# Performance work log

Hardware: AMD Instinct MI355X
Metric: run time of the kernel (lower is better)

## Reference

```python
import jax, jax.numpy as jnp
import numpy as np
import math

D_MODEL = 512
N_HEADS = 4
ANCHOR_PERIODS = [12, 24, 48, 96]
MIN_PERIOD = 4


def compute_periods(x, k=2, min_period=MIN_PERIOD):
    # x: [B, T, C] -> per-channel top-k ACF periods [C, k] (torch code runs this under no_grad)
    B, T, C = x.shape
    xc = x - x.mean(axis=1, keepdims=True)
    n_fft = 1 << (2 * T - 1).bit_length()
    xf = jnp.fft.rfft(xc, n=n_fft, axis=1)
    acf = jnp.fft.irfft(xf * jnp.conj(xf), n=n_fft, axis=1)[:, :T, :]
    avg = acf.mean(axis=0)  # [T, C]
    neg = jnp.array(-jnp.inf, avg.dtype)
    avg = avg.at[:min_period, :].set(neg)
    prev = jnp.roll(avg, 1, axis=0)
    nxt = jnp.roll(avg, -1, axis=0)
    is_peak = (avg > prev) & (avg > nxt) & (avg > 0)
    masked = jnp.where(is_peak, avg, neg)
    _, inds = jax.lax.top_k(masked.T, k)  # [C, k], top over lag axis
    return jnp.clip(inds, min_period, T // 2)


def _interp_matrix(new_len, old_len):
    # rows of F.interpolate(eye, size=(new_len, old_len), mode='bilinear', align_corners=False)
    j = np.arange(new_len, dtype=np.float64)
    src = np.clip((j + 0.5) * old_len / new_len - 0.5, 0.0, old_len - 1)
    i0 = np.floor(src).astype(np.int64)
    i1 = np.minimum(i0 + 1, old_len - 1)
    w = src - i0
    M = np.zeros((new_len, old_len), np.float32)
    M[np.arange(new_len), i0] += (1.0 - w).astype(np.float32)
    M[np.arange(new_len), i1] += w.astype(np.float32)
    return M


def flex_weight(anchors, target_len):
    nearest = min(ANCHOR_PERIODS, key=lambda p: abs(p - target_len))
    old = anchors[nearest]  # [d, nearest]
    if nearest == target_len:
        return old
    M = _interp_matrix(target_len, nearest)          # [new, old]
    Mpinv = jnp.asarray(np.linalg.pinv(M.T))          # pinv(resize_mat.T): [new, old]
    return (Mpinv @ old.T).T * math.sqrt(target_len / nearest)  # [d, new]


def attentive_agg(tokens, in_w, in_b, out_w, out_b, ln_g, ln_b):
    # tokens: [N, P, d]; MHA(query=last patch, key=value=all patches), eval mode (dropout=identity)
    N, P, d = tokens.shape
    hd = d // N_HEADS
    q = tokens[:, -1:, :]  # [N, 1, d]
    Wq, Wk, Wv = jnp.split(in_w, 3, axis=0)
    bq, bk, bv = jnp.split(in_b, 3)

    def heads(t, W, b):
        y = t @ W.T + b
        return y.reshape(N, t.shape[1], N_HEADS, hd).transpose(0, 2, 1, 3)

    Q = heads(q, Wq, bq)       # [N, H, 1, hd]
    K = heads(tokens, Wk, bk)  # [N, H, P, hd]
    V = heads(tokens, Wv, bv)
    attn = jax.nn.softmax(jnp.einsum('nhqe,nhke->nhqk', Q, K) / math.sqrt(hd), axis=-1)
    o = jnp.einsum('nhqk,nhke->nhqe', attn, V).transpose(0, 2, 1, 3).reshape(N, 1, d)
    o = o @ out_w.T + out_b
    y = q + o
    mu = y.mean(-1, keepdims=True)
    var = y.var(-1, keepdims=True)
    y = (y - mu) * jax.lax.rsqrt(var + 1e-5) * ln_g + ln_b
    return y[:, 0, :]


def setup_inputs() -> dict:
    key = jax.random.key(0)
    ks = jax.random.split(key, 16)
    B, T, C, d = 16, 384, 128, D_MODEL

    def xavier(k, shape):
        lim = math.sqrt(6.0 / (shape[0] + shape[1]))
        return jax.random.uniform(k, shape, jnp.float32, -lim, lim)

    inp = {'x': jax.random.normal(ks[0], (B, T, C), jnp.float32)}
    for i, p in enumerate(ANCHOR_PERIODS):
        inp[f'anchor_w{p}'] = xavier(ks[1 + i], (d, p))
    inp['shared_bias'] = jnp.zeros((d,), jnp.float32)
    for j, tag in enumerate(['agg1', 'agg2']):
        inp[f'{tag}_in_w'] = xavier(ks[5 + 2 * j], (3 * d, d))
        inp[f'{tag}_in_b'] = jnp.zeros((3 * d,), jnp.float32)
        inp[f'{tag}_out_w'] = xavier(ks[6 + 2 * j], (d, d))
        inp[f'{tag}_out_b'] = jnp.zeros((d,), jnp.float32)
        inp[f'{tag}_ln_g'] = jnp.ones((d,), jnp.float32)
        inp[f'{tag}_ln_b'] = jnp.zeros((d,), jnp.float32)
    inp['fusion_w1'] = xavier(ks[9], (d, 3 * d))
    inp['fusion_b1'] = jnp.zeros((d,), jnp.float32)
    inp['fusion_w2'] = xavier(ks[10], (d, d))
    inp['fusion_b2'] = jnp.zeros((d,), jnp.float32)
    return inp


def reference(x, anchor_w12, anchor_w24, anchor_w48, anchor_w96, shared_bias,
              agg1_in_w, agg1_in_b, agg1_out_w, agg1_out_b, agg1_ln_g, agg1_ln_b,
              agg2_in_w, agg2_in_b, agg2_out_w, agg2_out_b, agg2_ln_g, agg2_ln_b,
              fusion_w1, fusion_b1, fusion_w2, fusion_b2):
    B, T, C = x.shape
    d = D_MODEL
    periods = np.asarray(jax.device_get(compute_periods(x)))  # [C, 2] (no-grad routing)
    anchors = {12: anchor_w12, 24: anchor_w24, 48: anchor_w48, 96: anchor_w96}
    x_inv = jnp.transpose(x, (0, 2, 1))  # [B, C, T]

    w_trend = flex_weight(anchors, T)
    trend = x_inv @ w_trend.T + shared_bias  # [B, C, d]

    s1 = jnp.zeros((B, C, d), x.dtype)
    s2 = jnp.zeros((B, C, d), x.dtype)
    agg1 = (agg1_in_w, agg1_in_b, agg1_out_w, agg1_out_b, agg1_ln_g, agg1_ln_b)
    agg2 = (agg2_in_w, agg2_in_b, agg2_out_w, agg2_out_b, agg2_ln_g, agg2_ln_b)

    for p in np.unique(periods):
        p = int(p)
        m1 = periods[:, 0] == p
        m2 = periods[:, 1] == p
        tgt_idx = np.where(m1 | m2)[0]
        if tgt_idx.size == 0:
            continue
        w_p = flex_weight(anchors, p)
        num_p = T // p
        # unfold(size=p, step=p) == contiguous reshape of the first num_p*p samples
        patches = x_inv[:, tgt_idx, :num_p * p].reshape(B, tgt_idx.size, num_p, p)
        tokens = patches @ w_p.T + shared_bias  # [B, Csub, num_p, d]
        for m, aggp, slot in ((m1, agg1, 0), (m2, agg2, 1)):
            idx = np.where(m)[0]
            if idx.size == 0:
                continue
            rel = np.isin(tgt_idx, idx)
            sub = tokens[:, rel].reshape(-1, num_p, d)
            res = attentive_agg(sub, *aggp).reshape(B, idx.size, d)
            if slot == 0:
                s1 = s1.at[:, idx, :].set(res)
            else:
                s2 = s2.at[:, idx, :].set(res)

    combined = jnp.concatenate([s1, s2, trend], axis=-1)  # [B, C, 3d]
    h = jax.nn.gelu(combined @ fusion_w1.T + fusion_b1, approximate=False)
    return h @ fusion_w2.T + fusion_b2  # [B, C, d] (final dropout = identity in eval)
```

## Files before the change

kernel.cpp:

```cpp
#include <hip/hip_runtime.h>
#include <math.h>

#define Bn 16
#define Tn 384
#define Cn 128

static constexpr long OFF_XT   = 0;
static constexpr long OFF_AVG  = 786432;
static constexpr long OFF_PER  = 835584;
static constexpr long OFF_MP   = 835840;
static constexpr long OFF_AT   = 2507140;
static constexpr long OFF_WAF  = 2605444;
static constexpr long OFF_QAT  = 3195268;
static constexpr long OFF_VAT  = 3391876;
static constexpr long OFF_OVT  = 3588484;
static constexpr long OFF_CON  = 4374916;
static constexpr long OFF_VB   = 4377988;
static constexpr long OFF_MT   = 4379012;
static constexpr long OFF_DEF  = 4673924;
static constexpr long OFF_ZC   = 4677004;
static constexpr long OFF_COMB = 6643084;
static constexpr long OFF_H    = 9788812;
static constexpr long OFF_H2   = 10837388;
static constexpr long WS_FLOATS = 11885964;
// ... 307 lines not shown
      float v = part + inb[r];
      if (r < 1024) cons[s * 1536 + r] = v;
      else vbuf[s * 512 + (r - 1024)] = v;
    }
  }
}

__global__ __launch_bounds__(256) void prep1(const float* __restrict__ a12,
                                             const float* __restrict__ a24,
                                             const float* __restrict__ a48,
                                             const float* __restrict__ a96,
                                             const float* __restrict__ i1w,
                                             const float* __restrict__ i1b,
                                             const float* __restrict__ i2w,
                                             const float* __restrict__ i2b,
                                             const float* __restrict__ sb,
                                             float* __restrict__ at_tab,
                                             float* __restrict__ cons,
                                             float* __restrict__ vbuf) {
  __shared__ float sm[64 * 97];
  int bid = blockIdx.x;
  if (bid < 32) at_body(bid, a12, a24, a48, a96, at_tab, sm);
  else constsA_body(bid - 32, i1w, i1b, i2w, i2b, sb, cons, vbuf, sm);
}

__global__ __launch_bounds__(256) void wa_gemm2(const float* __restrict__ iw0,
                                                const float* __restrict__ iw1,
                                                const float* __restrict__ atb,
                                                float* __restrict__ waf,
                                                float* __restrict__ qat,
                                                float* __restrict__ vat) {
  __shared__ float smem[2 * 32 * 68];
  float* As = smem;
  float* Ws = smem + 32 * 68;
  int bid = blockIdx.x;
  int s = bid / 72, r = bid % 72;
  int m0 = (r / 3) * 64, n0 = (r % 3) * 64;
  const float* A = s ? iw1 : iw0;
  float* wafs = waf + (long)s * 294912;
  int tid = threadIdx.x;
  int tm = tid & 15, tn = tid >> 4;
  float acc[4][4];
#pragma unroll
  for (int i = 0; i < 4; ++i)
#pragma unroll
    for (int j = 0; j < 4; ++j) acc[i][j] = 0.f;
  int row = tid >> 3, kc = (tid & 7) * 4;
  for (int k0 = 0; k0 < 512; k0 += 32) {
    float4 v = *(const float4*)&A[(long)(m0 + row) * 512 + k0 + kc];
    As[(kc + 0) * 68 + row] = v.x; As[(kc + 1) * 68 + row] = v.y;
    As[(kc + 2) * 68 + row] = v.z; As[(kc + 3) * 68 + row] = v.w;
    v = *(const float4*)&A[(long)(m0 + row + 32) * 512 + k0 + kc];
    As[(kc + 0) * 68 + row + 32] = v.x; As[(kc + 1) * 68 + row + 32] = v.y;
    As[(kc + 2) * 68 + row + 32] = v.z; As[(kc + 3) * 68 + row + 32] = v.w;
    v = *(const float4*)&atb[(long)(n0 + row) * 512 + k0 + kc];
    Ws[(kc + 0) * 68 + row] = v.x; Ws[(kc + 1) * 68 + row] = v.y;
    Ws[(kc + 2) * 68 + row] = v.z; Ws[(kc + 3) * 68 + row] = v.w;
    v = *(const float4*)&atb[(long)(n0 + row + 32) * 512 + k0 + kc];
    Ws[(kc + 0) * 68 + row + 32] = v.x; Ws[(kc + 1) * 68 + row + 32] = v.y;
    Ws[(kc + 2) * 68 + row + 32] = v.z; Ws[(kc + 3) * 68 + row + 32] = v.w;
    __syncthreads();
    for (int kk = 0; kk < 32; ++kk) {
      float4 a = *(const float4*)&As[kk * 68 + tm * 4];
      float4 w = *(const float4*)&Ws[kk * 68 + tn * 4];
      acc[0][0] += a.x * w.x; acc[0][1] += a.x * w.y; acc[0][2] += a.x * w.z; acc[0][3] += a.x * w.w;
      acc[1][0] += a.y * w.x; acc[1][1] += a.y * w.y; acc[1][2] += a.y * w.z; acc[1][3] += a.y * w.w;
      acc[2][0] += a.z * w.x; acc[2][1] += a.z * w.y; acc[2][2] += a.z * w.z; acc[2][3] += a.z * w.w;
      acc[3][0] += a.w * w.x; acc[3][1] += a.w * w.y; acc[3][2] += a.w * w.z; acc[3][3] += a.w * w.w;
    }
    __syncthreads();
  }
#pragma unroll
  for (int mi = 0; mi < 4; ++mi) {
    float4 o;
    o.x = acc[mi][0]; o.y = acc[mi][1]; o.z = acc[mi][2]; o.w = acc[mi][3];
    *(float4*)&wafs[(long)(m0 + tm * 4 + mi) * 192 + n0 + tn * 4] = o;
  }
  if (m0 < 512 || m0 >= 1024) {
    float* Ct = smem;
#pragma unroll
    for (int mi = 0; mi < 4; ++mi)
#pragma unroll
      for (int j = 0; j < 4; ++j)
        Ct[(tn * 4 + j) * 65 + tm * 4 + mi] = acc[mi][j];
    __syncthreads();
    float* dst = ((m0 < 512) ? qat : vat) + (long)s * 98304;
    int mr = m0 & 511;
    for (int i = tid; i < 64 * 64; i += 256) {
      int cc = i >> 6, rr = i & 63;
      dst[(long)(n0 + cc) * 512 + mr + rr] = Ct[cc * 65 + rr];
    }
  }
}

__device__ void constsB_body(int bid, const float* __restrict__ o1w,
                             const float* __restrict__ o1b, const float* __restrict__ o2w,
                             const float* __restrict__ o2b, const float* __restrict__ vbuf,
                             float* __restrict__ cons, float* vv) {
  int s = bid / 32, r0 = (bid % 32) * 16;
  const float* outw = s ? o2w : o1w;
  const float* outb = s ? o2b : o1b;
  int tid = threadIdx.x;
  for (int i = tid; i < 512; i += 256) vv[i] = vbuf[s * 512 + i];
  __syncthreads();
  int lane = tid & 63, w = tid >> 6;
  for (int rr = 0; rr < 4; ++rr) {
    int r = r0 + w * 4 + rr;
    const float* row = outw + (long)r * 512;
    float part = 0.f;
    for (int kk = 0; kk < 8; ++kk) part += row[lane + 64 * kk] * vv[lane + 64 * kk];
    for (int off = 32; off > 0; off >>= 1) part += __shfl_down(part, off, 64);
    if (lane == 0) cons[s * 1536 + 1024 + r] = part + outb[r];
  }
}

__device__ void mt_body(int bid, const float* __restrict__ qat,
                        const float* __restrict__ waf, float* __restrict__ mt,
                        float* As, float* Ws) {
  int s4h = bid / 9, t = bid % 9;
  int s = s4h >> 2, h = s4h & 3;
  int m0 = (t / 3) * 64, n0 = (t % 3) * 64;
  const float* A = qat + (long)s * 98304 + h * 128;
  const float* B = waf + (long)s * 294912 + 98304 + (long)(h * 128) * 192;
  float* C = mt + (long)s4h * 36864;
  int tid = threadIdx.x;
  int tm = tid & 15, tn = tid >> 4;
  float acc[4][4];
#pragma unroll
  for (int i = 0; i < 4; ++i)
#pragma unroll
    for (int j = 0; j < 4; ++j) acc[i][j] = 0.f;
  int row = tid >> 3, kc = (tid & 7) * 4;
  for (int k0 = 0; k0 < 128; k0 += 32) {
    float4 v = *(const float4*)&A[(long)(m0 + row) * 512 + k0 + kc];
    As[(kc + 0) * 68 + row] = v.x; As[(kc + 1) * 68 + row] = v.y;
    As[(kc + 2) * 68 + row] = v.z; As[(kc + 3) * 68 + row] = v.w;
    v = *(const float4*)&A[(long)(m0 + row + 32) * 512 + k0 + kc];
    As[(kc + 0) * 68 + row + 32] = v.x; As[(kc + 1) * 68 + row + 32] = v.y;
    As[(kc + 2) * 68 + row + 32] = v.z; As[(kc + 3) * 68 + row + 32] = v.w;
    for (int l = tid; l < 512; l += 256) {
      int i = l >> 4, kq = (l & 15) * 4;
      float4 b = *(const float4*)&B[(long)(k0 + i) * 192 + n0 + kq];
      Ws[i * 68 + kq + 0] = b.x; Ws[i * 68 + kq + 1] = b.y;
      Ws[i * 68 + kq + 2] = b.z; Ws[i * 68 + kq + 3] = b.w;
    }
    __syncthreads();
    for (int kk = 0; kk < 32; ++kk) {
      float4 a = *(const float4*)&As[kk * 68 + tm * 4];
      float4 w = *(const float4*)&Ws[kk * 68 + tn * 4];
      acc[0][0] += a.x * w.x; acc[0][1] += a.x * w.y; acc[0][2] += a.x * w.z; acc[0][3] += a.x * w.w;
      acc[1][0] += a.y * w.x; acc[1][1] += a.y * w.y; acc[1][2] += a.y * w.z; acc[1][3] += a.y * w.w;
      acc[2][0] += a.z * w.x; acc[2][1] += a.z * w.y; acc[2][2] += a.z * w.z; acc[2][3] += a.z * w.w;
      acc[3][0] += a.w * w.x; acc[3][1] += a.w * w.y; acc[3][2] += a.w * w.z; acc[3][3] += a.w * w.w;
    }
    __syncthreads();
  }
#pragma unroll
  for (int mi = 0; mi < 4; ++mi) {
    float4 o;
    o.x = acc[mi][0]; o.y = acc[mi][1]; o.z = acc[mi][2]; o.w = acc[mi][3];
    *(float4*)&C[(long)(m0 + tm * 4 + mi) * 192 + n0 + tn * 4] = o;
  }
}

__device__ void sc_body(int bid, const float* __restrict__ qat,
                        const float* __restrict__ waf, const float* __restrict__ cons,
                        float* __restrict__ def, float* qcl, float* kbl) {
  int s = bid >> 2, h = bid & 3;
  int tid = threadIdx.x;
  const float* qc = cons + s * 1536;
  const float* kb = qc + 512;
  if (tid < 128) {
    qcl[tid] = qc[h * 128 + tid];
    kbl[tid] = kb[h * 128 + tid];
  }
  __syncthreads();
  const float* katb = waf + (long)s * 294912 + 98304;
  const float* qats = qat + (long)s * 98304;
  float* dtab = def + (long)(s * 4 + h) * 192;
  float* etab = def + 1536 + (long)(s * 4 + h) * 192;
  float* ftab = def + 3072 + (s * 4 + h);
  if (tid < 192) {
    float acc = 0.f;
    for (int i = 0; i < 128; ++i) acc += katb[(long)(h * 128 + i) * 192 + tid] * qcl[i];
    dtab[tid] = acc;
    float acc2 = 0.f;
    const float* qr = qats + (long)tid * 512 + h * 128;
    for (int i = 0; i < 128; ++i) acc2 += qr[i] * kbl[i];
    etab[tid] = acc2;
  }
  if (tid < 64) {
    float acc = 0.f;
    for (int i = tid; i < 128; i += 64) acc += qcl[i] * kbl[i];
    for (int off = 32; off > 0; off >>= 1) acc += __shfl_down(acc, off, 64);
    if (tid == 0) *ftab = acc;
  }
}

__device__ void ova_body(int bid, const float* __restrict__ ow0,
                         const float* __restrict__ ow1, const float* __restrict__ vat,
                         float* __restrict__ ovt, float* As, float* Ws) {
  int s = bid / 96, r = bid % 96;
  int h = r / 24, r2 = r % 24;
  int m0 = (r2 / 8) * 64, n0 = (r2 % 8) * 64;
  const float* A = vat + (long)s * 98304 + h * 128;
  const float* W = (s ? ow1 : ow0) + h * 128;
  float* C = ovt + ((long)(s * 4 + h) * 192) * 512;
  int tid = threadIdx.x;
  int tm = tid & 15, tn = tid >> 4;
  float acc[4][4];
#pragma unroll
  for (int i = 0; i < 4; ++i)
#pragma unroll
    for (int j = 0; j < 4; ++j) acc[i][j] = 0.f;
  int row = tid >> 3, kc = (tid & 7) * 4;
  for (int k0 = 0; k0 < 128; k0 += 32) {
    float4 v = *(const float4*)&A[(long)(m0 + row) * 512 + k0 + kc];
    As[(kc + 0) * 68 + row] = v.x; As[(kc + 1) * 68 + row] = v.y;
    As[(kc + 2) * 68 + row] = v.z; As[(kc + 3) * 68 + row] = v.w;
    v = *(const float4*)&A[(long)(m0 + row + 32) * 512 + k0 + kc];
    As[(kc + 0) * 68 + row + 32] = v.x; As[(kc + 1) * 68 + row + 32] = v.y;
    As[(kc + 2) * 68 + row + 32] = v.z; As[(kc + 3) * 68 + row + 32] = v.w;
    v = *(const float4*)&W[(long)(n0 + row) * 512 + k0 + kc];
    Ws[(kc + 0) * 68 + row] = v.x; Ws[(kc + 1) * 68 + row] = v.y;
    Ws[(kc + 2) * 68 + row] = v.z; Ws[(kc + 3) * 68 + row] = v.w;
    v = *(const float4*)&W[(long)(n0 + row + 32) * 512 + k0 + kc];
    Ws[(kc + 0) * 68 + row + 32] = v.x; Ws[(kc + 1) * 68 + row + 32] = v.y;
    Ws[(kc + 2) * 68 + row + 32] = v.z; Ws[(kc + 3) * 68 + row + 32] = v.w;
    __syncthreads();
    for (int kk = 0; kk < 32; ++kk) {
      float4 a = *(const float4*)&As[kk * 68 + tm * 4];
      float4 w = *(const float4*)&Ws[kk * 68 + tn * 4];
      acc[0][0] += a.x * w.x; acc[0][1] += a.x * w.y; acc[0][2] += a.x * w.z; acc[0][3] += a.x * w.w;
      acc[1][0] += a.y * w.x; acc[1][1] += a.y * w.y; acc[1][2] += a.y * w.z; acc[1][3] += a.y * w.w;
      acc[2][0] += a.z * w.x; acc[2][1] += a.z * w.y; acc[2][2] += a.z * w.z; acc[2][3] += a.z * w.w;
      acc[3][0] += a.w * w.x; acc[3][1] += a.w * w.y; acc[3][2] += a.w * w.z; acc[3][3] += a.w * w.w;
    }
    __syncthreads();
  }
#pragma unroll
  for (int mi = 0; mi < 4; ++mi) {
    float4 o;
    o.x = acc[mi][0]; o.y = acc[mi][1]; o.z = acc[mi][2]; o.w = acc[mi][3];
    *(float4*)&C[(long)(m0 + tm * 4 + mi) * 512 + n0 + tn * 4] = o;
  }
}

__global__ __launch_bounds__(256) void prep2(const float* __restrict__ o1w,
                                             const float* __restrict__ o1b,
                                             const float* __restrict__ o2w,
                                             const float* __restrict__ o2b,
                                             const float* __restrict__ vbuf,
                                             float* __restrict__ cons,
                                             const float* __restrict__ qat,
                                             const float* __restrict__ waf,
                                             float* __restrict__ mtab,
                                             float* __restrict__ def,
                                             const float* __restrict__ vat,
                                             float* __restrict__ ovt) {
  __shared__ float sm[2 * 32 * 68];
  int bid = blockIdx.x;
  if (bid < 64) constsB_body(bid, o1w, o1b, o2w, o2b, vbuf, cons, sm);
  else if (bid < 136) mt_body(bid - 64, qat, waf, mtab, sm, sm + 32 * 68);
  else if (bid < 144) sc_body(bid - 136, qat, waf, cons, def, sm, sm + 128);
  else ova_body(bid - 144, o1w, o2w, vat, ovt, sm, sm + 32 * 68);
}

__global__ __launch_bounds__(256) void attn_a(
    const float* __restrict__ xT, const int* __restrict__ per,
    const float* __restrict__ mp, const float* __restrict__ mt,
    const float* __restrict__ def, float* __restrict__ zc) {
  __shared__ float xb[8 * 384];
  __shared__ float Z[8 * 1248];
  __shared__ float zl[8 * 96];
  __shared__ float arb[8 * 384];
  __shared__ float qkc[32];
  float* scp = xb;

  int tid = threadIdx.x;
  int bid = blockIdx.x;
  int slot = bid & 1;
  int c = (bid >> 1) & 127;
  int b0 = (bid >> 8) * 8;
  int p = per[c * 2 + slot];
  int n = nanch(p);
  int np = Tn / p;
  int n1 = n + 1;
  float s = sqrtf((float)p / (float)n);
  float s2 = s * s;
  const float rscale = 0.08838834764831845f;
  int pre = apre(n);
  const float* mpp = mp + mpoff(p);
  const float* dt = def + (long)(slot * 4) * 192;
  const float* et = def + 1536 + (long)(slot * 4) * 192;
  const float* ft = def + 3072 + slot * 4;
  const float* mtb = mt + (long)(slot * 4) * 36864;

  for (int g = 0; g < 8; ++g)
    for (int t = tid; t < Tn; t += 256)
      xb[g * 384 + t] = xT[((long)c * Bn + b0 + g) * Tn + t];
  __syncthreads();

  {
    int half = n >> 1;
    int tot1 = np * half;
    for (int idx = tid; idx < tot1; idx += 256) {
      int j = idx / half, k2 = idx - j * half;
      int k = k2 * 2;
      int jb = j * p;
      const float* mk = mpp + k;
      float a0[8], a1[8];
#pragma unroll
      for (int g = 0; g < 8; ++g) { a0[g] = 0.f; a1[g] = 0.f; }
      for (int t = 0; t < p; ++t) {
        float2 m = *(const float2*)&mk[(long)t * n];
#pragma unroll
        for (int g = 0; g < 8; ++g) {
          float xv = xb[g * 384 + jb + t];
          a0[g] += m.x * xv;
          a1[g] += m.y * xv;
        }
      }
      int zi = j * n1 + k;
#pragma unroll
      for (int g = 0; g < 8; ++g) {
        Z[g * 1248 + zi] = a0[g];
        Z[g * 1248 + zi + 1] = a1[g];
      }
    }
  }
  __syncthreads();

  for (int idx = tid; idx < 8 * n; idx += 256) {
    int g = idx / n, k = idx - g * n;
    zl[g * 96 + k] = Z[g * 1248 + (np - 1) * n1 + k];
  }
  __syncthreads();

  {
    int pair = tid >> 3, l = tid & 7;
    int g = pair >> 2, h = pair & 3;
    const float* eh = et + h * 192 + pre;
    float acc = 0.f;
    for (int j = l; j < n; j += 8) acc += eh[j] * zl[g * 96 + j];
    for (int off = 4; off > 0; off >>= 1) acc += __shfl_down(acc, off, 8);
    if (l == 0) qkc[g * 4 + h] = s * acc + ft[h];
  }
  {
    int tot = 4 * n;
    for (int idx = tid; idx < tot; idx += 256) {
      int h = idx / n, k = idx - h * n;
      const float* mtc = mtb + (long)h * 36864 + (long)pre * 192 + pre + k;
      float a[8];
#pragma unroll
      for (int g = 0; g < 8; ++g) a[g] = 0.f;
      for (int j0 = 0; j0 < n; j0 += 4) {
        float4 zb[8];
#pragma unroll
        for (int g = 0; g < 8; ++g) zb[g] = *(const float4*)&zl[g * 96 + j0];
#pragma unroll
        for (int c4 = 0; c4 < 4; ++c4) {
          float mv = mtc[(long)(j0 + c4) * 192];
#pragma unroll
          for (int g = 0; g < 8; ++g) {
            float zv = (c4 == 0) ? zb[g].x : (c4 == 1) ? zb[g].y : (c4 == 2) ? zb[g].z : zb[g].w;
            a[g] += mv * zv;
          }
        }
      }
      float dv = dt[h * 192 + pre + k];
#pragma unroll
      for (int g = 0; g < 8; ++g) arb[g * 384 + h * 96 + k] = s2 * a[g] + s * dv;
    }
  }
  __syncthreads();

  {
    int fnp = 4 * np;
    int tot = 8 * fnp;
    for (int idx = tid; idx < tot; idx += 256) {
      int g = idx / fnp;
      int r = idx - g * fnp;
      int h = r / np, j = r - h * np;
      const float* ap = arb + g * 384 + h * 96;
      const float* zp = Z + g * 1248 + j * n1;
      float acc = 0.f;
      for (int k = 0; k < n; ++k) acc += ap[k] * zp[k];
      scp[g * 384 + h * np + j] = (acc + qkc[g * 4 + h]) * rscale;
    }
  }
  __syncthreads();

  {
    int pair = tid >> 3, l = tid & 7;
    int g = pair >> 2, h = pair & 3;
    float* sp = scp + g * 384 + h * np;
    float m = -1e30f;
    for (int j = l; j < np; j += 8) m = fmaxf(m, sp[j]);
    for (int off = 4; off > 0; off >>= 1) m = fmaxf(m, __shfl_xor(m, off, 8));
    float lsum = 0.f;
    for (int j = l; j < np; j += 8) { float e = expf(sp[j] - m); sp[j] = e; lsum += e; }
    for (int off = 4; off > 0; off >>= 1) lsum += __shfl_xor(lsum, off, 8);
    float il = 1.f / lsum;
    for (int j = l; j < np; j += 8) sp[j] *= il;
  }
  __syncthreads();

  {
    int fn = 4 * n;
    int tot = 8 * fn;
    for (int idx = tid; idx < tot; idx += 256) {
      int g = idx / fn;
      int r = idx - g * fn;
      int h = r / n, k = r - h * n;
      const float* sp = scp + g * 384 + h * np;
      const float* zp = Z + g * 1248 + k;
      float acc = 0.f;
      for (int j = 0; j < np; ++j) acc += sp[j] * zp[j * n1];
      arb[g * 384 + h * 96 + k] = acc;
    }
  }
  __syncthreads();

  {
    long rowb = ((long)slot * 128 + c) * 16 + b0;
    int fn5 = 5 * n;
    int tot = 8 * fn5;
    for (int idx = tid; idx < tot; idx += 256) {
      int g = idx / fn5, r = idx - g * fn5;
      int seg = r / n, k = r - seg * n;
      float v = (seg == 0) ? zl[g * 96 + k] : arb[g * 384 + (seg - 1) * 96 + k];
      zc[(rowb + g) * 480 + seg * 96 + k] = s * v;
    }
  }
}

__global__ __launch_bounds__(256) void attn_y(
    const int* __restrict__ per, const float* __restrict__ zc,
    const float* __restrict__ at_tab, const float* __restrict__ ovt,
    const float* __restrict__ cons, const float* __restrict__ sb,
    const float* __restrict__ l1g, const float* __restrict__ l1b,
    const float* __restrict__ l2g, const float* __restrict__ l2b,
    float* __restrict__ comb) {
  __shared__ float zbuf[16 * 480];
  __shared__ float red[128];
  __shared__ float stats[32];
  int tid = threadIdx.x;
  int bid = blockIdx.x;
  int slot = bid & 1, c = bid >> 1;
  int p = per[c * 2 + slot];
  int n = nanch(p);
  int pre = apre(n);
  const float* atb = at_tab + (long)pre * 512;
  const float* oc = cons + slot * 1536 + 1024;
  const float* lng = slot ? l2g : l1g;
  const float* lnb = slot ? l2b : l1b;
  long rowb = ((long)slot * 128 + c) * 16;
  int fn5 = 5 * n;
  for (int idx = tid; idx < 16 * fn5; idx += 256) {
    int g = idx / fn5, r = idx - g * fn5;
    int seg = r / n, k = r - seg * n;
    zbuf[g * 480 + seg * 96 + k] = zc[(rowb + g) * 480 + seg * 96 + k];
  }
  __syncthreads();
  int d0 = 2 * tid;
  float acc0[16], acc1[16];
#pragma unroll
  for (int r = 0; r < 16; ++r) { acc0[r] = 0.f; acc1[r] = 0.f; }
  for (int seg = 0; seg < 5; ++seg) {
    const float* wt = (seg == 0) ? atb
                                 : (ovt + ((long)(slot * 4 + seg - 1) * 192 + pre) * 512);
    int zoff = seg * 96;
    for (int k0 = 0; k0 < n; k0 += 4) {
      float4 zv[16];
#pragma unroll
      for (int r = 0; r < 16; ++r) zv[r] = *(const float4*)&zbuf[r * 480 + zoff + k0];
#pragma unroll
      for (int c4 = 0; c4 < 4; ++c4) {
        float2 w = *(const float2*)&wt[(long)(k0 + c4) * 512 + d0];
#pragma unroll
        for (int r = 0; r < 16; ++r) {
          float z = (c4 == 0) ? zv[r].x : (c4 == 1) ? zv[r].y : (c4 == 2) ? zv[r].z : zv[r].w;
          acc0[r] += w.x * z;
          acc1[r] += w.y * z;
        }
      }
    }
  }
  float2 sbv = *(const float2*)&sb[d0];
  float2 ocv = *(const float2*)&oc[d0];
  float s0 = sbv.x + ocv.x, s1 = sbv.y + ocv.y;
#pragma unroll
  for (int r = 0; r < 16; ++r) { acc0[r] += s0; acc1[r] += s1; }
  float ps[32];
#pragma unroll
  for (int r = 0; r < 16; ++r) {
    ps[2 * r] = acc0[r] + acc1[r];
    ps[2 * r + 1] = acc0[r] * acc0[r] + acc1[r] * acc1[r];
  }
  int w = tid >> 6, lane = tid & 63;
  for (int off = 32; off > 0; off >>= 1) {
#pragma unroll
    for (int i = 0; i < 32; ++i) ps[i] += __shfl_down(ps[i], off, 64);
  }
  if (lane == 0) {
#pragma unroll
    for (int i = 0; i < 32; ++i) red[w * 32 + i] = ps[i];
  }
  __syncthreads();
  if (tid < 16) {
    int r = tid;
    float ssum = red[2 * r] + red[32 + 2 * r] + red[64 + 2 * r] + red[96 + 2 * r];
    float qsum = red[2 * r + 1] + red[32 + 2 * r + 1] + red[64 + 2 * r + 1] + red[96 + 2 * r + 1];
    float mu = ssum / 512.f;
    float var = qsum / 512.f - mu * mu;
    stats[2 * r] = mu;
    stats[2 * r + 1] = rsqrtf(var + 1e-5f);
  }
  __syncthreads();
  float2 gv = *(const float2*)&lng[d0];
  float2 bv = *(const float2*)&lnb[d0];
#pragma unroll
  for (int r = 0; r < 16; ++r) {
    float mu = stats[2 * r], rstd = stats[2 * r + 1];
    long base = ((long)r * Cn + c) * 1536 + slot * 512;
    float2 o;
    o.x = (acc0[r] - mu) * rstd * gv.x + bv.x;
    o.y = (acc1[r] - mu) * rstd * gv.y + bv.y;
    *(float2*)&comb[base + d0] = o;
  }
}

__global__ __launch_bounds__(256) void trend_kernel(const float* __restrict__ xT,
                                                    const float* __restrict__ mp384,
                                                    const float* __restrict__ at96,
                                                    const float* __restrict__ sb,
                                                    float* __restrict__ comb) {
  __shared__ float xb[Bn * Tn];
  __shared__ float Ztr[Bn * 97];
  int c = blockIdx.x, tid = threadIdx.x;
  for (int i = tid; i < Bn * Tn; i += 256) xb[i] = xT[(long)c * Bn * Tn + i];
  __syncthreads();
  for (int idx = tid; idx < 4 * 96; idx += 256) {
    int bq = idx / 96, k = idx - bq * 96;
    const float* x0 = xb + (bq * 4 + 0) * Tn;
    const float* x1 = xb + (bq * 4 + 1) * Tn;
    const float* x2 = xb + (bq * 4 + 2) * Tn;
    const float* x3 = xb + (bq * 4 + 3) * Tn;
    const float* mk = mp384 + k;
    float a0 = 0.f, a1 = 0.f, a2 = 0.f, a3 = 0.f;
    for (int t = 0; t < Tn; ++t) {
      float m = mk[(long)t * 96];
      a0 += m * x0[t]; a1 += m * x1[t]; a2 += m * x2[t]; a3 += m * x3[t];
    }
    Ztr[(bq * 4 + 0) * 97 + k] = a0;
    Ztr[(bq * 4 + 1) * 97 + k] = a1;
    Ztr[(bq * 4 + 2) * 97 + k] = a2;
    Ztr[(bq * 4 + 3) * 97 + k] = a3;
  }
  __syncthreads();
  float acc0[Bn], acc1[Bn];
#pragma unroll
  for (int b = 0; b < Bn; ++b) { acc0[b] = 0.f; acc1[b] = 0.f; }
  for (int k = 0; k < 96; ++k) {
    float w0 = at96[(long)k * 512 + tid];
    float w1 = at96[(long)k * 512 + 256 + tid];
#pragma unroll
    for (int b = 0; b < Bn; ++b) {
      float z = Ztr[b * 97 + k];
      acc0[b] += w0 * z;
      acc1[b] += w1 * z;
    }
  }
  float s0 = sb[tid], s1 = sb[256 + tid];
#pragma unroll
  for (int b = 0; b < Bn; ++b) {
    long base = ((long)b * Cn + c) * 1536 + 1024;
    comb[base + tid] = 2.f * acc0[b] + s0;
    comb[base + 256 + tid] = 2.f * acc1[b] + s1;
  }
}

__global__ __launch_bounds__(256) void gemm1_part(const float* __restrict__ A,
                                                  const float* __restrict__ W,
                                                  float* __restrict__ C0,
                                                  float* __restrict__ C1) {
  __shared__ float As[32 * 68];
  __shared__ float Ws[32 * 68];
  int bid = blockIdx.x;
  int kh = bid >> 8;
  int r = bid & 255;
  int m0 = (r >> 3) * 64, n0 = (r & 7) * 64;
  float* C = kh ? C1 : C0;
  const float* Ab = A + kh * 768;
  const float* Wb = W + kh * 768;
  int tid = threadIdx.x;
  int tm = tid & 15, tn = tid >> 4;
  float acc[4][4];
#pragma unroll
  for (int i = 0; i < 4; ++i)
#pragma unroll
    for (int j = 0; j < 4; ++j) acc[i][j] = 0.f;
  int row = tid >> 3, kc = (tid & 7) * 4;
  for (int k0 = 0; k0 < 768; k0 += 32) {
    float4 v = *(const float4*)&Ab[(long)(m0 + row) * 1536 + k0 + kc];
    As[(kc + 0) * 68 + row] = v.x; As[(kc + 1) * 68 + row] = v.y;
    As[(kc + 2) * 68 + row] = v.z; As[(kc + 3) * 68 + row] = v.w;
    v = *(const float4*)&Ab[(long)(m0 + row + 32) * 1536 + k0 + kc];
    As[(kc + 0) * 68 + row + 32] = v.x; As[(kc + 1) * 68 + row + 32] = v.y;
    As[(kc + 2) * 68 + row + 32] = v.z; As[(kc + 3) * 68 + row + 32] = v.w;
    v = *(const float4*)&Wb[(long)(n0 + row) * 1536 + k0 + kc];
    Ws[(kc + 0) * 68 + row] = v.x; Ws[(kc + 1) * 68 + row] = v.y;
    Ws[(kc + 2) * 68 + row] = v.z; Ws[(kc + 3) * 68 + row] = v.w;
    v = *(const float4*)&Wb[(long)(n0 + row + 32) * 1536 + k0 + kc];
    Ws[(kc + 0) * 68 + row + 32] = v.x; Ws[(kc + 1) * 68 + row + 32] = v.y;
    Ws[(kc + 2) * 68 + row + 32] = v.z; Ws[(kc + 3) * 68 + row + 32] = v.w;
    __syncthreads();
    for (int kk = 0; kk < 32; ++kk) {
      float4 a = *(const float4*)&As[kk * 68 + tm * 4];
      float4 w = *(const float4*)&Ws[kk * 68 + tn * 4];
      acc[0][0] += a.x * w.x; acc[0][1] += a.x * w.y; acc[0][2] += a.x * w.z; acc[0][3] += a.x * w.w;
      acc[1][0] += a.y * w.x; acc[1][1] += a.y * w.y; acc[1][2] += a.y * w.z; acc[1][3] += a.y * w.w;
      acc[2][0] += a.z * w.x; acc[2][1] += a.z * w.y; acc[2][2] += a.z * w.z; acc[2][3] += a.z * w.w;
      acc[3][0] += a.w * w.x; acc[3][1] += a.w * w.y; acc[3][2] += a.w * w.z; acc[3][3] += a.w * w.w;
    }
    __syncthreads();
  }
#pragma unroll
  for (int mi = 0; mi < 4; ++mi) {
    float4 o;
    o.x = acc[mi][0]; o.y = acc[mi][1]; o.z = acc[mi][2]; o.w = acc[mi][3];
    *(float4*)&C[(long)(m0 + tm * 4 + mi) * 512 + n0 + tn * 4] = o;
  }
}

__global__ __launch_bounds__(256) void gelu_red(float* __restrict__ H,
                                                const float* __restrict__ H2,
                                                const float* __restrict__ fb1) {
  int i = blockIdx.x * 256 + threadIdx.x;
  float4 a = ((const float4*)H)[i];
  float4 b = ((const float4*)H2)[i];
  int col4 = (i & 127) << 2;
  float4 bs = *(const float4*)&fb1[col4];
  float4 v;
  v.x = a.x + b.x + bs.x;
  v.y = a.y + b.y + bs.y;
  v.z = a.z + b.z + bs.z;
  v.w = a.w + b.w + bs.w;
  v.x = 0.5f * v.x * (1.f + erff(v.x * 0.7071067811865475f));
  v.y = 0.5f * v.y * (1.f + erff(v.y * 0.7071067811865475f));
  v.z = 0.5f * v.z * (1.f + erff(v.z * 0.7071067811865475f));
  v.w = 0.5f * v.w * (1.f + erff(v.w * 0.7071067811865475f));
  ((float4*)H)[i] = v;
}

template <bool GELU>
__global__ __launch_bounds__(256) void fused_gemm(const float* __restrict__ A,
                                                  const float* __restrict__ W,
                                                  const float* __restrict__ bias,
                                                  float* __restrict__ C,
                                                  int N, int K) {
  __shared__ float As[32 * 68];
  __shared__ float Ws[32 * 68];
  int nb = N >> 6;
  int m0 = (blockIdx.x / nb) * 64, n0 = (blockIdx.x % nb) * 64;
  int tid = threadIdx.x;
  int tm = tid & 15, tn = tid >> 4;
  float acc[4][4];
#pragma unroll
  for (int i = 0; i < 4; ++i)
#pragma unroll
    for (int j = 0; j < 4; ++j) acc[i][j] = 0.f;
  int row = tid >> 3, kc = (tid & 7) * 4;
  for (int k0 = 0; k0 < K; k0 += 32) {
    {
      float4 v = *(const float4*)&A[(long)(m0 + row) * K + k0 + kc];
      As[(kc + 0) * 68 + row] = v.x; As[(kc + 1) * 68 + row] = v.y;
      As[(kc + 2) * 68 + row] = v.z; As[(kc + 3) * 68 + row] = v.w;
      v = *(const float4*)&A[(long)(m0 + row + 32) * K + k0 + kc];
      As[(kc + 0) * 68 + row + 32] = v.x; As[(kc + 1) * 68 + row + 32] = v.y;
      As[(kc + 2) * 68 + row + 32] = v.z; As[(kc + 3) * 68 + row + 32] = v.w;
      v = *(const float4*)&W[(long)(n0 + row) * K + k0 + kc];
      Ws[(kc + 0) * 68 + row] = v.x; Ws[(kc + 1) * 68 + row] = v.y;
      Ws[(kc + 2) * 68 + row] = v.z; Ws[(kc + 3) * 68 + row] = v.w;
      v = *(const float4*)&W[(long)(n0 + row + 32) * K + k0 + kc];
      Ws[(kc + 0) * 68 + row + 32] = v.x; Ws[(kc + 1) * 68 + row + 32] = v.y;
      Ws[(kc + 2) * 68 + row + 32] = v.z; Ws[(kc + 3) * 68 + row + 32] = v.w;
    }
    __syncthreads();
    for (int kk = 0; kk < 32; ++kk) {
      float4 a = *(const float4*)&As[kk * 68 + tm * 4];
      float4 w = *(const float4*)&Ws[kk * 68 + tn * 4];
      acc[0][0] += a.x * w.x; acc[0][1] += a.x * w.y; acc[0][2] += a.x * w.z; acc[0][3] += a.x * w.w;
      acc[1][0] += a.y * w.x; acc[1][1] += a.y * w.y; acc[1][2] += a.y * w.z; acc[1][3] += a.y * w.w;
      acc[2][0] += a.z * w.x; acc[2][1] += a.z * w.y; acc[2][2] += a.z * w.z; acc[2][3] += a.z * w.w;
      acc[3][0] += a.w * w.x; acc[3][1] += a.w * w.y; acc[3][2] += a.w * w.z; acc[3][3] += a.w * w.w;
    }
    __syncthreads();
  }
  float b0v = bias[n0 + tn * 4 + 0], b1v = bias[n0 + tn * 4 + 1];
  float b2v = bias[n0 + tn * 4 + 2], b3v = bias[n0 + tn * 4 + 3];
#pragma unroll
  for (int mi = 0; mi < 4; ++mi) {
    float4 o;
    o.x = acc[mi][0] + b0v; o.y = acc[mi][1] + b1v;
    o.z = acc[mi][2] + b2v; o.w = acc[mi][3] + b3v;
    if (GELU) {
      o.x = 0.5f * o.x * (1.f + erff(o.x * 0.7071067811865475f));
      o.y = 0.5f * o.y * (1.f + erff(o.y * 0.7071067811865475f));
      o.z = 0.5f * o.z * (1.f + erff(o.z * 0.7071067811865475f));
      o.w = 0.5f * o.w * (1.f + erff(o.w * 0.7071067811865475f));
    }
    *(float4*)&C[(long)(m0 + tm * 4 + mi) * N + n0 + tn * 4] = o;
  }
}

extern "C" void kernel_launch(void* const* d_in, const int* in_sizes, int n_in,
                              void* d_out, int out_size, void* d_ws, size_t ws_size,
                              hipStream_t stream) {
  const float* x    = (const float*)d_in[0];
  const float* a12  = (const float*)d_in[1];
  const float* a24  = (const float*)d_in[2];
  const float* a48  = (const float*)d_in[3];
  const float* a96  = (const float*)d_in[4];
  const float* sb   = (const float*)d_in[5];
  const float* g1iw = (const float*)d_in[6];
  const float* g1ib = (const float*)d_in[7];
  const float* g1ow = (const float*)d_in[8];
  const float* g1ob = (const float*)d_in[9];
  const float* g1lg = (const float*)d_in[10];
  const float* g1lb = (const float*)d_in[11];
  const float* g2iw = (const float*)d_in[12];
  const float* g2ib = (const float*)d_in[13];
  const float* g2ow = (const float*)d_in[14];
  const float* g2ob = (const float*)d_in[15];
  const float* g2lg = (const float*)d_in[16];
  const float* g2lb = (const float*)d_in[17];
  const float* fw1  = (const float*)d_in[18];
  const float* fb1  = (const float*)d_in[19];
  const float* fw2  = (const float*)d_in[20];
  const float* fb2  = (const float*)d_in[21];

  if (ws_size < (size_t)WS_FLOATS * sizeof(float)) return;

  float* ws   = (float*)d_ws;
  float* xT   = ws + OFF_XT;
  float* avg  = ws + OFF_AVG;
  int*   per  = (int*)(ws + OFF_PER);
  float* mp   = ws + OFF_MP;
  float* atb  = ws + OFF_AT;
  float* waf  = ws + OFF_WAF;
  float* qat  = ws + OFF_QAT;
  float* vat  = ws + OFF_VAT;
  float* ovt  = ws + OFF_OVT;
  float* cons = ws + OFF_CON;
  float* vbuf = ws + OFF_VB;
  float* mtab = ws + OFF_MT;
  float* def  = ws + OFF_DEF;
  float* zc   = ws + OFF_ZC;
  float* comb = ws + OFF_COMB;
  float* hbuf = ws + OFF_H;
  float* hbu2 = ws + OFF_H2;
  float* out  = (float*)d_out;

  transpose_kernel<<<192, 256, 0, stream>>>(x, xT);
  acf_kernel<<<Cn * 6, 256, 0, stream>>>(xT, avg);
  periods_kernel<<<32, 256, 0, stream>>>(avg, per);
  build_mpinv_kernel<<<190, 256, 0, stream>>>(per, mp);
  prep1<<<224, 256, 0, stream>>>(a12, a24, a48, a96, g1iw, g1ib, g2iw, g2ib, sb,
                                 atb, cons, vbuf);
  wa_gemm2<<<144, 256, 0, stream>>>(g1iw, g2iw, atb, waf, qat, vat);
  prep2<<<336, 256, 0, stream>>>(g1ow, g1ob, g2ow, g2ob, vbuf, cons,
                                 qat, waf, mtab, def, vat, ovt);
  attn_a<<<512, 256, 0, stream>>>(xT, per, mp, mtab, def, zc);
  attn_y<<<256, 256, 0, stream>>>(per, zc, atb, ovt, cons, sb,
                                  g1lg, g1lb, g2lg, g2lb, comb);
  trend_kernel<<<Cn, 256, 0, stream>>>(xT, mp + 1634436L, atb + 84L * 512, sb, comb);
  gemm1_part<<<512, 256, 0, stream>>>(comb, fw1, hbuf, hbu2);
  gelu_red<<<1024, 256, 0, stream>>>(hbuf, hbu2, fb1);
  fused_gemm<false><<<256, 256, 0, stream>>>(hbuf, fw2, fb2, out, 512, 512);
}
```

Before: 440.7 us.

## Retile attn_a projection, double-buffer gemm1, fuse GELU reduction into gemm2

Three separate changes. The attn_a projection loop is retiled so each thread computes 16 output columns for 2 batch rows using float4 loads of the Mpinv matrix instead of 2 columns for 8 rows, which cuts redundant matrix loads. gemm1_part gains a double-buffered LDS pipeline that prefetches the next K-chunk into registers while the current one is computed. The separate gelu_red kernel is removed and its split-K sum, bias and GELU are folded into the A-tile load of the second GEMM, saving one launch and one full read/write pass over H. In exchange the attn_a retile raises register pressure and the fused gemm2 recomputes erf for each of its 8 column blocks.

```diff
diff --git a/kernel.cpp b/kernel.cpp
--- a/kernel.cpp
+++ b/kernel.cpp
@@ -633,31 +633,40 @@
   __syncthreads();
 
   {
-    int half = n >> 1;
-    int tot1 = np * half;
-    for (int idx = tid; idx < tot1; idx += 256) {
-      int j = idx / half, k2 = idx - j * half;
-      int k = k2 * 2;
+    int nkc = (n + 15) >> 4;
+    int items = np * nkc * 4;
+    for (int idx = tid; idx < items; idx += 256) {
+      int gg = idx & 3;
+      int t4 = idx >> 2;
+      int j = t4 / nkc, kc_ = t4 - j * nkc;
+      int k0 = kc_ * 16;
       int jb = j * p;
-      const float* mk = mpp + k;
-      float a0[8], a1[8];
-#pragma unroll
-      for (int g = 0; g < 8; ++g) { a0[g] = 0.f; a1[g] = 0.f; }
+      const float* xr0 = xb + (gg * 2) * 384 + jb;
+      const float* xr1 = xr0 + 384;
+      const float* mrow = mpp + k0;
+      float a0[16], a1[16];
+#pragma unroll
+      for (int e = 0; e < 16; ++e) { a0[e] = 0.f; a1[e] = 0.f; }
       for (int t = 0; t < p; ++t) {
-        float2 m = *(const float2*)&mk[(long)t * n];
-#pragma unroll
-        for (int g = 0; g < 8; ++g) {
-          float xv = xb[g * 384 + jb + t];
-          a0[g] += m.x * xv;
-          a1[g] += m.y * xv;
-        }
+        float x0 = xr0[t], x1 = xr1[t];
+        const float* mr = mrow + (long)t * n;
+        float4 m0 = *(const float4*)&mr[0];
+        float4 m1 = *(const float4*)&mr[4];
+        float4 m2 = *(const float4*)&mr[8];
+        float4 m3 = *(const float4*)&mr[12];
+        a0[0] += m0.x * x0;  a0[1] += m0.y * x0;  a0[2] += m0.z * x0;  a0[3] += m0.w * x0;
+        a0[4] += m1.x * x0;  a0[5] += m1.y * x0;  a0[6] += m1.z * x0;  a0[7] += m1.w * x0;
+        a0[8] += m2.x * x0;  a0[9] += m2.y * x0;  a0[10] += m2.z * x0; a0[11] += m2.w * x0;
+        a0[12] += m3.x * x0; a0[13] += m3.y * x0; a0[14] += m3.z * x0; a0[15] += m3.w * x0;
+        a1[0] += m0.x * x1;  a1[1] += m0.y * x1;  a1[2] += m0.z * x1;  a1[3] += m0.w * x1;
+        a1[4] += m1.x * x1;  a1[5] += m1.y * x1;  a1[6] += m1.z * x1;  a1[7] += m1.w * x1;
+        a1[8] += m2.x * x1;  a1[9] += m2.y * x1;  a1[10] += m2.z * x1; a1[11] += m2.w * x1;
+        a1[12] += m3.x * x1; a1[13] += m3.y * x1; a1[14] += m3.z * x1; a1[15] += m3.w * x1;
       }
-      int zi = j * n1 + k;
-#pragma unroll
-      for (int g = 0; g < 8; ++g) {
-        Z[g * 1248 + zi] = a0[g];
-        Z[g * 1248 + zi + 1] = a1[g];
-      }
+      int kcnt = min(16, n - k0);
+      float* z0 = Z + (gg * 2) * 1248 + j * n1 + k0;
+      float* z1 = z0 + 1248;
+      for (int e = 0; e < kcnt; ++e) { z0[e] = a0[e]; z1[e] = a1[e]; }
     }
   }
   __syncthreads();
@@ -916,8 +925,8 @@
                                                   const float* __restrict__ W,
                                                   float* __restrict__ C0,
                                                   float* __restrict__ C1) {
-  __shared__ float As[32 * 68];
-  __shared__ float Ws[32 * 68];
+  __shared__ float As[2][32 * 68];
+  __shared__ float Ws[2][32 * 68];
   int bid = blockIdx.x;
   int kh = bid >> 8;
   int r = bid & 255;
@@ -927,25 +936,105 @@
   const float* Wb = W + kh * 768;
   int tid = threadIdx.x;
   int tm = tid & 15, tn = tid >> 4;
+  int row = tid >> 3, kc = (tid & 7) * 4;
+  float acc[4][4];
+#pragma unroll
+  for (int i = 0; i < 4; ++i)
+#pragma unroll
+    for (int j = 0; j < 4; ++j) acc[i][j] = 0.f;
+  float4 ra0, ra1, rw0, rw1;
+  auto ld = [&](int k0) {
+    ra0 = *(const float4*)&Ab[(long)(m0 + row) * 1536 + k0 + kc];
+    ra1 = *(const float4*)&Ab[(long)(m0 + row + 32) * 1536 + k0 + kc];
+    rw0 = *(const float4*)&Wb[(long)(n0 + row) * 1536 + k0 + kc];
+    rw1 = *(const float4*)&Wb[(long)(n0 + row + 32) * 1536 + k0 + kc];
+  };
+  auto st = [&](int b) {
+    float* as = As[b]; float* ws = Ws[b];
+    as[(kc + 0) * 68 + row] = ra0.x; as[(kc + 1) * 68 + row] = ra0.y;
+    as[(kc + 2) * 68 + row] = ra0.z; as[(kc + 3) * 68 + row] = ra0.w;
+    as[(kc + 0) * 68 + row + 32] = ra1.x; as[(kc + 1) * 68 + row + 32] = ra1.y;
+    as[(kc + 2) * 68 + row + 32] = ra1.z; as[(kc + 3) * 68 + row + 32] = ra1.w;
+    ws[(kc + 0) * 68 + row] = rw0.x; ws[(kc + 1) * 68 + row] = rw0.y;
+    ws[(kc + 2) * 68 + row] = rw0.z; ws[(kc + 3) * 68 + row] = rw0.w;
+    ws[(kc + 0) * 68 + row + 32] = rw1.x; ws[(kc + 1) * 68 + row + 32] = rw1.y;
+    ws[(kc + 2) * 68 + row + 32] = rw1.z; ws[(kc + 3) * 68 + row + 32] = rw1.w;
+  };
+  ld(0); st(0); __syncthreads();
+  ld(32);
+  for (int ch = 0; ch < 24; ++ch) {
+    int cur = ch & 1;
+    const float* as = As[cur];
+    const float* ws = Ws[cur];
+    for (int kk = 0; kk < 32; ++kk) {
+      float4 a = *(const float4*)&as[kk * 68 + tm * 4];
+      float4 w = *(const float4*)&ws[kk * 68 + tn * 4];
+      acc[0][0] += a.x * w.x; acc[0][1] += a.x * w.y; acc[0][2] += a.x * w.z; acc[0][3] += a.x * w.w;
+      acc[1][0] += a.y * w.x; acc[1][1] += a.y * w.y; acc[1][2] += a.y * w.z; acc[1][3] += a.y * w.w;
+      acc[2][0] += a.z * w.x; acc[2][1] += a.z * w.y; acc[2][2] += a.z * w.z; acc[2][3] += a.z * w.w;
+      acc[3][0] += a.w * w.x; acc[3][1] += a.w * w.y; acc[3][2] += a.w * w.z; acc[3][3] += a.w * w.w;
+    }
+    __syncthreads();
+    if (ch + 1 < 24) {
+      st(cur ^ 1);
+      if (ch + 2 < 24) ld((ch + 2) * 32);
+      __syncthreads();
+    }
+  }
+#pragma unroll
+  for (int mi = 0; mi < 4; ++mi) {
+    float4 o;
+    o.x = acc[mi][0]; o.y = acc[mi][1]; o.z = acc[mi][2]; o.w = acc[mi][3];
+    *(float4*)&C[(long)(m0 + tm * 4 + mi) * 512 + n0 + tn * 4] = o;
+  }
+}
+
+__global__ __launch_bounds__(256) void gemm2_fused(const float* __restrict__ H0,
+                                                   const float* __restrict__ H1,
+                                                   const float* __restrict__ fb1,
+                                                   const float* __restrict__ W,
+                                                   const float* __restrict__ fb2,
+                                                   float* __restrict__ C) {
+  __shared__ float As[32 * 68];
+  __shared__ float Ws[32 * 68];
+  int m0 = (blockIdx.x >> 3) * 64, n0 = (blockIdx.x & 7) * 64;
+  int tid = threadIdx.x;
+  int tm = tid & 15, tn = tid >> 4;
   float acc[4][4];
 #pragma unroll
   for (int i = 0; i < 4; ++i)
 #pragma unroll
     for (int j = 0; j < 4; ++j) acc[i][j] = 0.f;
   int row = tid >> 3, kc = (tid & 7) * 4;
-  for (int k0 = 0; k0 < 768; k0 += 32) {
-    float4 v = *(const float4*)&Ab[(long)(m0 + row) * 1536 + k0 + kc];
+  for (int k0 = 0; k0 < 512; k0 += 32) {
+    float4 bs = *(const float4*)&fb1[k0 + kc];
+    float4 h0 = *(const float4*)&H0[(long)(m0 + row) * 512 + k0 + kc];
+    float4 h1 = *(const float4*)&H1[(long)(m0 + row) * 512 + k0 + kc];
+    float4 v;
+    v.x = h0.x + h1.x + bs.x; v.y = h0.y + h1.y + bs.y;
+    v.z = h0.z + h1.z + bs.z; v.w = h0.w + h1.w + bs.w;
+    v.x = 0.5f * v.x * (1.f + erff(v.x * 0.7071067811865475f));
+    v.y = 0.5f * v.y * (1.f + erff(v.y * 0.7071067811865475f));
+    v.z = 0.5f * v.z * (1.f + erff(v.z * 0.7071067811865475f));
+    v.w = 0.5f * v.w * (1.f + erff(v.w * 0.7071067811865475f));
     As[(kc + 0) * 68 + row] = v.x; As[(kc + 1) * 68 + row] = v.y;
     As[(kc + 2) * 68 + row] = v.z; As[(kc + 3) * 68 + row] = v.w;
-    v = *(const float4*)&Ab[(long)(m0 + row + 32) * 1536 + k0 + kc];
+    h0 = *(const float4*)&H0[(long)(m0 + row + 32) * 512 + k0 + kc];
+    h1 = *(const float4*)&H1[(long)(m0 + row + 32) * 512 + k0 + kc];
+    v.x = h0.x + h1.x + bs.x; v.y = h0.y + h1.y + bs.y;
+    v.z = h0.z + h1.z + bs.z; v.w = h0.w + h1.w + bs.w;
+    v.x = 0.5f * v.x * (1.f + erff(v.x * 0.7071067811865475f));
+    v.y = 0.5f * v.y * (1.f + erff(v.y * 0.7071067811865475f));
+    v.z = 0.5f * v.z * (1.f + erff(v.z * 0.7071067811865475f));
+    v.w = 0.5f * v.w * (1.f + erff(v.w * 0.7071067811865475f));
     As[(kc + 0) * 68 + row + 32] = v.x; As[(kc + 1) * 68 + row + 32] = v.y;
     As[(kc + 2) * 68 + row + 32] = v.z; As[(kc + 3) * 68 + row + 32] = v.w;
-    v = *(const float4*)&Wb[(long)(n0 + row) * 1536 + k0 + kc];
-    Ws[(kc + 0) * 68 + row] = v.x; Ws[(kc + 1) * 68 + row] = v.y;
-    Ws[(kc + 2) * 68 + row] = v.z; Ws[(kc + 3) * 68 + row] = v.w;
-    v = *(const float4*)&Wb[(long)(n0 + row + 32) * 1536 + k0 + kc];
-    Ws[(kc + 0) * 68 + row + 32] = v.x; Ws[(kc + 1) * 68 + row + 32] = v.y;
-    Ws[(kc + 2) * 68 + row + 32] = v.z; Ws[(kc + 3) * 68 + row + 32] = v.w;
+    float4 wv = *(const float4*)&W[(long)(n0 + row) * 512 + k0 + kc];
+    Ws[(kc + 0) * 68 + row] = wv.x; Ws[(kc + 1) * 68 + row] = wv.y;
+    Ws[(kc + 2) * 68 + row] = wv.z; Ws[(kc + 3) * 68 + row] = wv.w;
+    wv = *(const float4*)&W[(long)(n0 + row + 32) * 512 + k0 + kc];
+    Ws[(kc + 0) * 68 + row + 32] = wv.x; Ws[(kc + 1) * 68 + row + 32] = wv.y;
+    Ws[(kc + 2) * 68 + row + 32] = wv.z; Ws[(kc + 3) * 68 + row + 32] = wv.w;
     __syncthreads();
     for (int kk = 0; kk < 32; ++kk) {
       float4 a = *(const float4*)&As[kk * 68 + tm * 4];
@@ -957,92 +1046,14 @@
     }
     __syncthreads();
   }
-#pragma unroll
-  for (int mi = 0; mi < 4; ++mi) {
-    float4 o;
-    o.x = acc[mi][0]; o.y = acc[mi][1]; o.z = acc[mi][2]; o.w = acc[mi][3];
-    *(float4*)&C[(long)(m0 + tm * 4 + mi) * 512 + n0 + tn * 4] = o;
-  }
-}
-
-__global__ __launch_bounds__(256) void gelu_red(float* __restrict__ H,
-                                                const float* __restrict__ H2,
-                                                const float* __restrict__ fb1) {
-  int i = blockIdx.x * 256 + threadIdx.x;
-  float4 a = ((const float4*)H)[i];
-  float4 b = ((const float4*)H2)[i];
-  int col4 = (i & 127) << 2;
-  float4 bs = *(const float4*)&fb1[col4];
-  float4 v;
-  v.x = a.x + b.x + bs.x;
-  v.y = a.y + b.y + bs.y;
-  v.z = a.z + b.z + bs.z;
-  v.w = a.w + b.w + bs.w;
-  v.x = 0.5f * v.x * (1.f + erff(v.x * 0.7071067811865475f));
-  v.y = 0.5f * v.y * (1.f + erff(v.y * 0.7071067811865475f));
-  v.z = 0.5f * v.z * (1.f + erff(v.z * 0.7071067811865475f));
-  v.w = 0.5f * v.w * (1.f + erff(v.w * 0.7071067811865475f));
-  ((float4*)H)[i] = v;
-}
-
-template <bool GELU>
-__global__ __launch_bounds__(256) void fused_gemm(const float* __restrict__ A,
-                                                  const float* __restrict__ W,
-                                                  const float* __restrict__ bias,
-                                                  float* __restrict__ C,
-                                                  int N, int K) {
-  __shared__ float As[32 * 68];
-  __shared__ float Ws[32 * 68];
-  int nb = N >> 6;
-  int m0 = (blockIdx.x / nb) * 64, n0 = (blockIdx.x % nb) * 64;
-  int tid = threadIdx.x;
-  int tm = tid & 15, tn = tid >> 4;
-  float acc[4][4];
-#pragma unroll
-  for (int i = 0; i < 4; ++i)
-#pragma unroll
-    for (int j = 0; j < 4; ++j) acc[i][j] = 0.f;
-  int row = tid >> 3, kc = (tid & 7) * 4;
-  for (int k0 = 0; k0 < K; k0 += 32) {
-    {
-      float4 v = *(const float4*)&A[(long)(m0 + row) * K + k0 + kc];
-      As[(kc + 0) * 68 + row] = v.x; As[(kc + 1) * 68 + row] = v.y;
-      As[(kc + 2) * 68 + row] = v.z; As[(kc + 3) * 68 + row] = v.w;
-      v = *(const float4*)&A[(long)(m0 + row + 32) * K + k0 + kc];
-      As[(kc + 0) * 68 + row + 32] = v.x; As[(kc + 1) * 68 + row + 32] = v.y;
-      As[(kc + 2) * 68 + row + 32] = v.z; As[(kc + 3) * 68 + row + 32] = v.w;
-      v = *(const float4*)&W[(long)(n0 + row) * K + k0 + kc];
-      Ws[(kc + 0) * 68 + row] = v.x; Ws[(kc + 1) * 68 + row] = v.y;
-      Ws[(kc + 2) * 68 + row] = v.z; Ws[(kc + 3) * 68 + row] = v.w;
-      v = *(const float4*)&W[(long)(n0 + row + 32) * K + k0 + kc];
-      Ws[(kc + 0) * 68 + row + 32] = v.x; Ws[(kc + 1) * 68 + row + 32] = v.y;
-      Ws[(kc + 2) * 68 + row + 32] = v.z; Ws[(kc + 3) * 68 + row + 32] = v.w;
-    }
-    __syncthreads();
-    for (int kk = 0; kk < 32; ++kk) {
-      float4 a = *(const float4*)&As[kk * 68 + tm * 4];
-      float4 w = *(const float4*)&Ws[kk * 68 + tn * 4];
-      acc[0][0] += a.x * w.x; acc[0][1] += a.x * w.y; acc[0][2] += a.x * w.z; acc[0][3] += a.x * w.w;
-      acc[1][0] += a.y * w.x; acc[1][1] += a.y * w.y; acc[1][2] += a.y * w.z; acc[1][3] += a.y * w.w;
-      acc[2][0] += a.z * w.x; acc[2][1] += a.z * w.y; acc[2][2] += a.z * w.z; acc[2][3] += a.z * w.w;
-      acc[3][0] += a.w * w.x; acc[3][1] += a.w * w.y; acc[3][2] += a.w * w.z; acc[3][3] += a.w * w.w;
-    }
-    __syncthreads();
-  }
-  float b0v = bias[n0 + tn * 4 + 0], b1v = bias[n0 + tn * 4 + 1];
-  float b2v = bias[n0 + tn * 4 + 2], b3v = bias[n0 + tn * 4 + 3];
+  float b0v = fb2[n0 + tn * 4 + 0], b1v = fb2[n0 + tn * 4 + 1];
+  float b2v = fb2[n0 + tn * 4 + 2], b3v = fb2[n0 + tn * 4 + 3];
 #pragma unroll
   for (int mi = 0; mi < 4; ++mi) {
     float4 o;
     o.x = acc[mi][0] + b0v; o.y = acc[mi][1] + b1v;
     o.z = acc[mi][2] + b2v; o.w = acc[mi][3] + b3v;
-    if (GELU) {
-      o.x = 0.5f * o.x * (1.f + erff(o.x * 0.7071067811865475f));
-      o.y = 0.5f * o.y * (1.f + erff(o.y * 0.7071067811865475f));
-      o.z = 0.5f * o.z * (1.f + erff(o.z * 0.7071067811865475f));
-      o.w = 0.5f * o.w * (1.f + erff(o.w * 0.7071067811865475f));
-    }
-    *(float4*)&C[(long)(m0 + tm * 4 + mi) * N + n0 + tn * 4] = o;
+    *(float4*)&C[(long)(m0 + tm * 4 + mi) * 512 + n0 + tn * 4] = o;
   }
 }
 
@@ -1108,6 +1119,5 @@
                                   g1lg, g1lb, g2lg, g2lb, comb);
   trend_kernel<<<Cn, 256, 0, stream>>>(xT, mp + 1634436L, atb + 84L * 512, sb, comb);
   gemm1_part<<<512, 256, 0, stream>>>(comb, fw1, hbuf, hbu2);
-  gelu_red<<<1024, 256, 0, stream>>>(hbuf, hbu2, fb1);
-  fused_gemm<false><<<256, 256, 0, stream>>>(hbuf, fw2, fb2, out, 512, 512);
-}
+  gemm2_fused<<<256, 256, 0, stream>>>(hbuf, hbu2, fb1, fw2, fb2, out);
+}
```

Measured after the change: 496.0 us. 12.5% more time.
